# Kernel tuning notes

Measured on AMD Instinct MI355X. Metric: run time of the kernel, lower is better.

## Reference

```python
import jax, jax.numpy as jnp
from jax import lax
import numpy as np

TAO = 12   # lag stride
M = 7      # number of lags (m)


def setup_inputs() -> dict:
    key = jax.random.key(0)
    k1, k2, k3, k4, k5 = jax.random.split(key, 5)
    B, L, C, D = 32, 4096, 21, 512
    K = D // C            # kernels per channel = 24
    LO = D - C * K        # leftout channels = 8
    return {
        "x": jax.random.normal(k1, (B, L, C), jnp.float32),
        "conv_w": jax.random.normal(k2, (K, M + 1, 3), jnp.float32) * 0.2,
        "conv_b": jax.random.normal(k3, (K,), jnp.float32) * 0.02,
        "leftout_w": jax.random.normal(k4, (LO, M + 1, 3), jnp.float32) * 0.2,
        "leftout_b": jax.random.normal(k5, (LO,), jnp.float32) * 0.02,
    }


def _circ_conv(x_ncl, w_oik, b_o):
    # circular padding=1, kernel_size=3, stride 1 -> same length
    xp = jnp.pad(x_ncl, ((0, 0), (0, 0), (1, 1)), mode="wrap")
    y = lax.conv_general_dilated(xp, w_oik, (1,), "VALID",
                                 dimension_numbers=("NCW", "OIW", "NCW"))
    return y + b_o[None, :, None]


def reference(x, conv_w, conv_b, leftout_w, leftout_b):
    B, L, C = x.shape
    K = conv_w.shape[0]
    nv = L - M * TAO
    # lagged gather: ext[b, t, c, j] = x[b, m*tao + t - j*tao, c]
    t_idx = jnp.arange(M * TAO, L)                      # [nv]
    offs = jnp.arange(M + 1) * TAO                      # [m+1]
    idx = t_idx[:, None] - offs[None, :]                # [nv, m+1]
    ext = x[:, idx, :]                                  # [B, nv, m+1, C]
    ext = jnp.transpose(ext, (0, 1, 3, 2))              # [B, nv, C, m+1] (channel-major)
    # pad=True: zero-pad the first m*tao timesteps
    ext = jnp.pad(ext, ((0, 0), (M * TAO, 0), (0, 0), (0, 0)))  # [B, L, C, m+1]
    # per-channel chunks as a single batched conv: [B*C, m+1, L]
    xc = jnp.transpose(ext, (0, 2, 3, 1)).reshape(B * C, M + 1, L)
    y = _circ_conv(xc, conv_w, conv_b).reshape(B, C * K, L)      # [B, C*K, L]
    # leftout conv applied to the last channel's chunk only
    last = jnp.transpose(ext[:, :, C - 1, :], (0, 2, 1))         # [B, m+1, L]
    yl = _circ_conv(last, leftout_w, leftout_b)                  # [B, LO, L]
    out = jnp.concatenate([y, yl], axis=1)                       # [B, d_model, L]
    return jnp.transpose(out, (0, 2, 1))                         # [B, L, d_model]
```

## Files before the change

kernel.cpp:

```cpp
#include <hip/hip_runtime.h>

#define LL 4096
#define CC 21
#define TT 64
#define XSTR 151

typedef float v2f __attribute__((ext_vector_type(2)));
typedef float v4f __attribute__((ext_vector_type(4)));

__device__ __forceinline__ v2f fma2(v2f a, v2f b, v2f c) {
    return __builtin_elementwise_fma(a, b, c);
}

template<bool EDGE>
__device__ __forceinline__ void compute_item(
    const float* __restrict__ xrow, const float* __restrict__ wtc,
    const float* __restrict__ biasc, float* __restrict__ outp,
    int vo0, int d0, int tg, int t0)
{
    v2f acc[16][2];
    {
        v2f b0 = { biasc[vo0],     biasc[vo0 + 1] };
        v2f b1 = { biasc[vo0 + 2], biasc[vo0 + 3] };
        #pragma unroll
        for (int ti = 0; ti < 16; ++ti) { acc[ti][0] = b0; acc[ti][1] = b1; }
    }

    bool msk[18];
    if (EDGE) {
        #pragma unroll
        for (int s = 0; s < 18; ++s)
            msk[s] = (((t0 + tg * 16 + s - 1) & (LL - 1)) < 84);
    }

    const int base = tg * 16 + 84;

    #pragma unroll 1
    for (int j = 0; j < 8; ++j) {
        const float* wp = &wtc[(3 * j) * 32 + vo0];
        float4 w0 = *reinterpret_cast<const float4*>(wp);
        float4 w1 = *reinterpret_cast<const float4*>(wp + 32);
        float4 w2 = *reinterpret_cast<const float4*>(wp + 64);

        const float* vp = xrow + base - 12 * j;
        float v[18];
        #pragma unroll
        for (int s = 0; s < 18; ++s) {
            float t = vp[s];
            if (EDGE && msk[s]) t = 0.0f;
            v[s] = t;
        }

        #pragma unroll
        for (int ti = 0; ti < 16; ++ti) {
            v2f vv, w;
            vv.x = vv.y = v[ti];
            w.x = w0.x; w.y = w0.y; acc[ti][0] = fma2(vv, w, acc[ti][0]);
            w.x = w0.z; w.y = w0.w; acc[ti][1] = fma2(vv, w, acc[ti][1]);
            vv.x = vv.y = v[ti + 1];
            w.x = w1.x; w.y = w1.y; acc[ti][0] = fma2(vv, w, acc[ti][0]);
            w.x = w1.z; w.y = w1.w; acc[ti][1] = fma2(vv, w, acc[ti][1]);
            vv.x = vv.y = v[ti + 2];
            w.x = w2.x; w.y = w2.y; acc[ti][0] = fma2(vv, w, acc[ti][0]);
            w.x = w2.z; w.y = w2.w; acc[ti][1] = fma2(vv, w, acc[ti][1]);
        }
    }

    #pragma unroll
    for (int ti = 0; ti < 16; ++ti) {
        v4f r = { acc[ti][0].x, acc[ti][0].y, acc[ti][1].x, acc[ti][1].y };
        float* p = outp + (size_t)(tg * 16 + ti) * 512 + d0;
        __builtin_nontemporal_store(r, reinterpret_cast<v4f*>(p));
    }
}

__global__ __launch_bounds__(256) void delay_fir_kernel(
    const float* __restrict__ x,
    const float* __restrict__ conv_w,
    const float* __restrict__ conv_b,
    const float* __restrict__ lw,
    const float* __restrict__ lb,
    float* __restrict__ out)
{
    __shared__ float xs[CC * XSTR];
    __shared__ __align__(16) float wtc[24 * 32];
    __shared__ float biasc[32];

    const int tid = threadIdx.x;
    const int t0 = blockIdx.x * TT;
    const int b  = blockIdx.y;

    for (int e = tid; e < 24 * 32; e += 256) {
        int jk = e >> 5, vo = e & 31;
        wtc[e] = (vo < 24) ? conv_w[vo * 24 + jk] : lw[(vo - 24) * 24 + jk];
    }
    if (tid < 32) biasc[tid] = (tid < 24) ? conv_b[tid] : lb[tid - 24];

    const float* xb = x + (size_t)b * (LL * CC);
    const int baset = t0 - 85;
    for (int e = tid; e < 150 * CC; e += 256) {
        int s = e / CC, c = e - s * CC;
        int time = (baset + s) & (LL - 1);
        xs[c * XSTR + s] = xb[time * CC + c];
    }
    __syncthreads();

    const int l = tid & 63;
    const int w = tid >> 6;
    const int h = w & 1;
    const int d0 = 256 * h + 4 * l;
    int c, vo0;
    if (d0 >= 504) { c = 20; vo0 = 24 + (d0 - 504); }
    else           { c = d0 / 24; vo0 = d0 - c * 24; }

    const float* xrow = &xs[c * XSTR];
    float* outp = out + ((size_t)b * LL + t0) * 512;
    const bool edge = (t0 == 0) | (t0 == TT) | (t0 == LL - TT);

    for (int it = 0; it < 2; ++it) {
        int tg = it * 2 + (w >> 1);
        if (edge) compute_item<true >(xrow, wtc, biasc, outp, vo0, d0, tg, t0);
        else      compute_item<false>(xrow, wtc, biasc, outp, vo0, d0, tg, t0);
    }
}

extern "C" void kernel_launch(void* const* d_in, const int* in_sizes, int n_in,
                              void* d_out, int out_size, void* d_ws, size_t ws_size,
                              hipStream_t stream) {
    const float* x      = (const float*)d_in[0];
    const float* conv_w = (const float*)d_in[1];
    const float* conv_b = (const float*)d_in[2];
    const float* lw     = (const float*)d_in[3];
    const float* lb     = (const float*)d_in[4];
    float* out = (float*)d_out;

    dim3 grid(LL / TT, 32);
    delay_fir_kernel<<<grid, 256, 0, stream>>>(x, conv_w, conv_b, lw, lb, out);
}
```

Baseline: 70.02 us.

## Make blocks persistent over four time tiles with double-buffered register-prefetched input staging

```diff
diff --git a/kernel.cpp b/kernel.cpp
--- a/kernel.cpp
+++ b/kernel.cpp
@@ -3,13 +3,41 @@
 #define LL 4096
 #define CC 21
 #define TT 64
+#define NTB 4
 #define XSTR 151
+#define STG_N (150 * CC)
+#define NSTG 13
 
 typedef float v2f __attribute__((ext_vector_type(2)));
 typedef float v4f __attribute__((ext_vector_type(4)));
 
 __device__ __forceinline__ v2f fma2(v2f a, v2f b, v2f c) {
     return __builtin_elementwise_fma(a, b, c);
+}
+
+__device__ __forceinline__ void prefetch_tile(const float* __restrict__ xb,
+                                              int baset, int tid, float* pf) {
+    const int lo21 = (0 - baset) * CC;
+    const int hi21 = (LL - baset) * CC;
+    #pragma unroll
+    for (int i = 0; i < NSTG; ++i) {
+        int e = tid + 256 * i;
+        if (e < STG_N) {
+            int ofs = baset * CC + e;
+            if (e < lo21)  ofs += LL * CC;
+            if (e >= hi21) ofs -= LL * CC;
+            pf[i] = xb[ofs];
+        }
+    }
+}
+
+__device__ __forceinline__ void write_tile(float* __restrict__ xsb, int tid,
+                                           const int* ldsoff, const float* pf) {
+    #pragma unroll
+    for (int i = 0; i < NSTG; ++i) {
+        int e = tid + 256 * i;
+        if (e < STG_N) xsb[ldsoff[i]] = pf[i];
+    }
 }
 
 template<bool EDGE>
@@ -82,13 +110,13 @@
     const float* __restrict__ lb,
     float* __restrict__ out)
 {
-    __shared__ float xs[CC * XSTR];
+    __shared__ float xs[2][CC * XSTR];
     __shared__ __align__(16) float wtc[24 * 32];
     __shared__ float biasc[32];
 
-    const int tid = threadIdx.x;
-    const int t0 = blockIdx.x * TT;
-    const int b  = blockIdx.y;
+    const int tid   = threadIdx.x;
+    const int b     = blockIdx.y;
+    const int tbase = blockIdx.x * (TT * NTB);
 
     for (int e = tid; e < 24 * 32; e += 256) {
         int jk = e >> 5, vo = e & 31;
@@ -97,30 +125,47 @@
     if (tid < 32) biasc[tid] = (tid < 24) ? conv_b[tid] : lb[tid - 24];
 
     const float* xb = x + (size_t)b * (LL * CC);
-    const int baset = t0 - 85;
-    for (int e = tid; e < 150 * CC; e += 256) {
-        int s = e / CC, c = e - s * CC;
-        int time = (baset + s) & (LL - 1);
-        xs[c * XSTR + s] = xb[time * CC + c];
+
+    int ldsoff[NSTG];
+    #pragma unroll
+    for (int i = 0; i < NSTG; ++i) {
+        int e = tid + 256 * i;
+        int s = e / CC, c2 = e - s * CC;
+        ldsoff[i] = c2 * XSTR + s;
     }
-    __syncthreads();
 
-    const int l = tid & 63;
-    const int w = tid >> 6;
-    const int h = w & 1;
-    const int d0 = 256 * h + 4 * l;
+    const int l  = tid & 63;
+    const int w  = tid >> 6;
+    const int d0 = 256 * (w & 1) + 4 * l;
     int c, vo0;
     if (d0 >= 504) { c = 20; vo0 = 24 + (d0 - 504); }
     else           { c = d0 / 24; vo0 = d0 - c * 24; }
 
-    const float* xrow = &xs[c * XSTR];
-    float* outp = out + ((size_t)b * LL + t0) * 512;
-    const bool edge = (t0 == 0) | (t0 == TT) | (t0 == LL - TT);
+    float pf[NSTG];
+    prefetch_tile(xb, tbase - 85, tid, pf);
+    write_tile(xs[0], tid, ldsoff, pf);
+    __syncthreads();
 
-    for (int it = 0; it < 2; ++it) {
-        int tg = it * 2 + (w >> 1);
-        if (edge) compute_item<true >(xrow, wtc, biasc, outp, vo0, d0, tg, t0);
-        else      compute_item<false>(xrow, wtc, biasc, outp, vo0, d0, tg, t0);
+    #pragma unroll 1
+    for (int tix = 0; tix < NTB; ++tix) {
+        const int t0 = tbase + tix * TT;
+        const float* xrow = &xs[tix & 1][c * XSTR];
+
+        if (tix + 1 < NTB) prefetch_tile(xb, t0 + TT - 85, tid, pf);
+
+        float* outp = out + ((size_t)b * LL + t0) * 512;
+        const bool edge = (t0 == 0) | (t0 == TT) | (t0 == LL - TT);
+        #pragma unroll 1
+        for (int it = 0; it < 2; ++it) {
+            int tg = it * 2 + (w >> 1);
+            if (edge) compute_item<true >(xrow, wtc, biasc, outp, vo0, d0, tg, t0);
+            else      compute_item<false>(xrow, wtc, biasc, outp, vo0, d0, tg, t0);
+        }
+
+        if (tix + 1 < NTB) {
+            write_tile(xs[(tix + 1) & 1], tid, ldsoff, pf);
+            __syncthreads();
+        }
     }
 }
 
@@ -134,6 +179,6 @@
     const float* lb     = (const float*)d_in[4];
     float* out = (float*)d_out;
 
-    dim3 grid(LL / TT, 32);
+    dim3 grid(LL / (TT * NTB), 32);
     delay_fir_kernel<<<grid, 256, 0, stream>>>(x, conv_w, conv_b, lw, lb, out);
 }
```

Result: faster. 64.23 us (-8.3%).
